# Kernel tuning notes

Hardware: AMD Instinct MI355X
Metric: run time of the kernel (lower is better)

Reference implementation:

```python
import jax, jax.numpy as jnp
import numpy as np

N = 50000   # nodes
D = 128     # hidden dim
E_NS = 250000  # non-self-loop edges
B = 4096    # sessions
NEG_SLOPE = 0.01  # F.leaky_relu default


def setup_inputs() -> dict:
    key = jax.random.key(0)
    ks = jax.random.split(key, 8)
    x = jax.random.normal(ks[0], (N, D), jnp.float32)
    src = jax.random.randint(ks[1], (E_NS,), 0, N)
    off = jax.random.randint(ks[2], (E_NS,), 1, N)
    dst = (src + off) % N  # guarantees src != dst
    loops = jnp.arange(N)
    edge_index = jnp.stack([jnp.concatenate([src, loops]),
                            jnp.concatenate([dst, loops])])  # [2, E_NS+N]
    batch = jnp.sort(jax.random.randint(ks[3], (N,), 0, B))
    local_sess_avg = jax.random.normal(ks[4], (B, D), jnp.float32)
    stdv = 1.0 / np.sqrt(D)
    W_alpha = jax.random.uniform(ks[5], (1, D), jnp.float32, -stdv, stdv)
    W_forward = jax.random.uniform(ks[6], (1, D), jnp.float32, -stdv, stdv)
    W_backward = jax.random.uniform(ks[7], (1, D), jnp.float32, -stdv, stdv)
    mt_sess_masks = jnp.ones((N,), jnp.int32)
    return {"x": x, "W_alpha": W_alpha, "W_forward": W_forward,
            "W_backward": W_backward, "local_sess_avg": local_sess_avg,
            "edge_index": edge_index, "batch": batch,
            "mt_sess_masks": mt_sess_masks, "n_nonself": E_NS}


def reference(x, W_alpha, W_forward, W_backward, local_sess_avg,
              edge_index, batch, mt_sess_masks, n_nonself):
    n = x.shape[0]
    src, dst = edge_index[0], edge_index[1]
    # non-self-loop edges occupy the first n_nonself columns (static int)
    src_ns, dst_ns = src[:n_nonself], dst[:n_nonself]
    # expanded edges = original edges + reversed non-self-loop edges
    exp_src = jnp.concatenate([src, dst_ns])  # [Et]
    exp_dst = jnp.concatenate([dst, src_ns])  # [Et]

    lrelu = lambda v: jax.nn.leaky_relu(v, NEG_SLOPE)

    exp_xi = x[exp_dst]                     # [Et, D]
    exp_xj = x[exp_src]                     # [Et, D]
    alpha_query = local_sess_avg[batch[exp_dst]]  # [Et, D]
    alpha = lrelu((exp_xi * alpha_query) @ W_alpha.T)        # [Et, 1]
    beta = lrelu((x[dst] * x[src]) @ W_forward.T)            # [E, 1]
    rbeta = lrelu((x[dst_ns] * x[src_ns]) @ W_backward.T)    # [E_ns, 1]
    logits = (jnp.concatenate([beta, rbeta], axis=0) + alpha)[:, 0]  # [Et]

    # segment softmax over target nodes (every node has a self-loop)
    seg_max = jax.lax.stop_gradient(
        jax.ops.segment_max(logits, exp_dst, num_segments=n))
    ex = jnp.exp(logits - seg_max[exp_dst])
    denom = jax.ops.segment_sum(ex, exp_dst, num_segments=n)
    aij = ex / denom[exp_dst]

    # scatter-add weighted neighbor features
    aggr = jax.ops.segment_sum(aij[:, None] * exp_xj, exp_dst, num_segments=n)

    # update: masked nodes take aggregate, others keep x; residual add
    new_x = jnp.where((mt_sess_masks == 1)[:, None], aggr, x)
    return new_x + x
```

## Files before the change

kernel.cpp:

```cpp
#include <hip/hip_runtime.h>

#define NEG_SLOPE 0.01f
#define STRIDE 32

__device__ __forceinline__ float lrelu(float v) { return v > 0.f ? v : NEG_SLOPE * v; }

__device__ __forceinline__ unsigned pack_bf16(float a, float b) {
    unsigned ua = __float_as_uint(a);
    ua = (ua + 0x7fffu + ((ua >> 16) & 1u)) >> 16;
    unsigned ub = __float_as_uint(b);
    ub = (ub + 0x7fffu + ((ub >> 16) & 1u)) & 0xffff0000u;
    return ua | ub;
}
__device__ __forceinline__ float blo(unsigned u) { return __uint_as_float(u << 16); }
__device__ __forceinline__ float bhi(unsigned u) { return __uint_as_float(u & 0xffff0000u); }

__device__ __forceinline__ void placeEdge(int s, int d, unsigned flag,
                                          int* __restrict__ cursor, int* __restrict__ slots) {
    int pos = atomicAdd(&cursor[d], 1);
    if (pos < STRIDE) slots[d * STRIDE + pos] = (int)((unsigned)s | flag);
}

__global__ void prep_kernel(const float4* __restrict__ x4, uint4* __restrict__ xh,
                            const int* __restrict__ EI0, const int* __restrict__ EI1,
                            int* __restrict__ cursor, int* __restrict__ slots,
                            int E_total, int E_NS, int nConvert) {
    int t = blockIdx.x * blockDim.x + threadIdx.x;
    if (t < nConvert) {
        float4 a = x4[2 * t], b = x4[2 * t + 1];
        uint4 o;
        o.x = pack_bf16(a.x, a.y);
        o.y = pack_bf16(a.z, a.w);
        o.z = pack_bf16(b.x, b.y);
        o.w = pack_bf16(b.z, b.w);
        xh[t] = o;
        return;
    }
    int u = t - nConvert;
    int n1v = E_total >> 2, n0v = E_NS >> 2;
    if (u < n1v) {
        int4 s = ((const int4*)EI0)[u];
        int4 d = ((const int4*)EI1)[u];
        placeEdge(s.x, d.x, 0u, cursor, slots);
        placeEdge(s.y, d.y, 0u, cursor, slots);
        placeEdge(s.z, d.z, 0u, cursor, slots);
        placeEdge(s.w, d.w, 0u, cursor, slots);
    } else if (u < n1v + n0v) {
        int v = u - n1v;
        int4 s = ((const int4*)EI1)[v];
        int4 d = ((const int4*)EI0)[v];
        placeEdge(s.x, d.x, 0x80000000u, cursor, slots);
        placeEdge(s.y, d.y, 0x80000000u, cursor, slots);
        placeEdge(s.z, d.z, 0x80000000u, cursor, slots);
        placeEdge(s.w, d.w, 0x80000000u, cursor, slots);
    } else if (u == n1v + n0v) {
        for (int e = E_total & ~3; e < E_total; e++)
            placeEdge(EI0[e], EI1[e], 0u, cursor, slots);
        for (int e = E_NS & ~3; e < E_NS; e++)
            placeEdge(EI1[e], EI0[e], 0x80000000u, cursor, slots);
    }
}

__device__ __forceinline__ float dot8u(uint4 h, float4 y0, float4 y1) {
    return blo(h.x) * y0.x + bhi(h.x) * y0.y + blo(h.y) * y0.z + bhi(h.y) * y0.w +
           blo(h.z) * y1.x + bhi(h.z) * y1.y + blo(h.w) * y1.z + bhi(h.w) * y1.w;
}

__global__ void gather_kernel(const float4* __restrict__ x4, const uint4* __restrict__ xh,
                              const float4* __restrict__ Wf4, const float4* __restrict__ Wb4,
                              const int* __restrict__ cursor, const int* __restrict__ slots,
                              const int* __restrict__ mask,
                              float4* __restrict__ out4, int N) {
    __shared__ int sbuck[16][STRIDE];
    int tid = blockIdx.x * blockDim.x + threadIdx.x;
    int node = tid >> 4;
    int sub = threadIdx.x & 15;
    int grp = threadIdx.x >> 4;
    bool active = (node < N);
    int nodeSafe = active ? node : 0;

    long long base = (long long)nodeSafe * 32;
    float4 xd0 = x4[base + 2 * sub];
    float4 xd1 = x4[base + 2 * sub + 1];
    int msk = active ? mask[nodeSafe] : 0;
    int cnt = (active && msk == 1) ? min(cursor[nodeSafe], STRIDE) : 0;

    if (sub < 8) ((int4*)sbuck[grp])[sub] = ((const int4*)slots)[(long long)nodeSafe * 8 + sub];

    float4 wf0 = Wf4[2 * sub], wf1 = Wf4[2 * sub + 1];
    float4 wb0 = Wb4[2 * sub], wb1 = Wb4[2 * sub + 1];
    float4 yf0 = {xd0.x * wf0.x, xd0.y * wf0.y, xd0.z * wf0.z, xd0.w * wf0.w};
    float4 yf1 = {xd1.x * wf1.x, xd1.y * wf1.y, xd1.z * wf1.z, xd1.w * wf1.w};
    float4 yb0 = {xd0.x * wb0.x, xd0.y * wb0.y, xd0.z * wb0.z, xd0.w * wb0.w};
    float4 yb1 = {xd1.x * wb1.x, xd1.y * wb1.y, xd1.z * wb1.z, xd1.w * wb1.w};

    int cm = cnt;
    cm = max(cm, __shfl_xor(cm, 16, 64));
    cm = max(cm, __shfl_xor(cm, 32, 64));

    float l = 0.f;
    float4 O0 = {0.f, 0.f, 0.f, 0.f}, O1 = {0.f, 0.f, 0.f, 0.f};

    for (int r = 0; r < cm; r += 8) {
        int e[8];
        uint4 h[8];
#pragma unroll
        for (int j = 0; j < 8; j++) {
            int i = r + j;
            e[j] = (i < cnt) ? sbuck[grp][i] : 0;
        }
#pragma unroll
        for (int j = 0; j < 8; j++)
            h[j] = xh[(long long)(e[j] & 0x7fffffff) * 16 + sub];

        float p[8];
#pragma unroll
        for (int j = 0; j < 8; j++) {
            float pf = dot8u(h[j], yf0, yf1);
            float pb = dot8u(h[j], yb0, yb1);
            p[j] = (e[j] < 0) ? pb : pf;
        }
#pragma unroll
        for (int sh = 1; sh < 16; sh <<= 1) {
#pragma unroll
            for (int j = 0; j < 8; j++) p[j] += __shfl_xor(p[j], sh, 64);
        }
#pragma unroll
        for (int j = 0; j < 8; j++) {
            float ev = (r + j < cnt) ? __expf(lrelu(p[j])) : 0.f;
            l += ev;
            O0.x += ev * blo(h[j].x); O0.y += ev * bhi(h[j].x);
            O0.z += ev * blo(h[j].y); O0.w += ev * bhi(h[j].y);
            O1.x += ev * blo(h[j].z); O1.y += ev * bhi(h[j].z);
            O1.z += ev * blo(h[j].w); O1.w += ev * bhi(h[j].w);
        }
    }

    if (active) {
        float4 ra, rb;
        if (msk == 1) {
            float inv = (l > 0.f) ? 1.f / l : 0.f;
            ra = {O0.x * inv + xd0.x, O0.y * inv + xd0.y, O0.z * inv + xd0.z, O0.w * inv + xd0.w};
            rb = {O1.x * inv + xd1.x, O1.y * inv + xd1.y, O1.z * inv + xd1.z, O1.w * inv + xd1.w};
        } else {
            ra = {2.f * xd0.x, 2.f * xd0.y, 2.f * xd0.z, 2.f * xd0.w};
            rb = {2.f * xd1.x, 2.f * xd1.y, 2.f * xd1.z, 2.f * xd1.w};
        }
        out4[base + 2 * sub] = ra;
        out4[base + 2 * sub + 1] = rb;
    }
}

extern "C" void kernel_launch(void* const* d_in, const int* in_sizes, int n_in,
                              void* d_out, int out_size, void* d_ws, size_t ws_size,
                              hipStream_t stream) {
    const float* x   = (const float*)d_in[0];
    const float* Wf  = (const float*)d_in[2];
    const float* Wb  = (const float*)d_in[3];
    const int* EI    = (const int*)d_in[5];
    const int* mask  = (const int*)d_in[7];

    int N = in_sizes[6];
    int E_total = in_sizes[5] / 2;
    int E_NS = E_total - N;

    const int* EI0 = EI;
    const int* EI1 = EI + E_total;

    char* ws = (char*)d_ws;
    int* cursor = (int*)ws;
    int* slots  = (int*)(ws + (size_t)N * 4);
    uint4* xh   = (uint4*)(ws + (size_t)N * 4 * (1 + STRIDE));

    hipMemsetAsync(cursor, 0, (size_t)N * 4, stream);

    const int BLK = 256;
    int nConvert = N * 16;
    int fillThreads = (E_total >> 2) + (E_NS >> 2) + 1;
    int prepBlocks = (nConvert + fillThreads + BLK - 1) / BLK;
    int nodeBlocks = ((N * 16) + BLK - 1) / BLK;

    prep_kernel<<<prepBlocks, BLK, 0, stream>>>((const float4*)x, xh, EI0, EI1,
                                                cursor, slots, E_total, E_NS, nConvert);
    gather_kernel<<<nodeBlocks, BLK, 0, stream>>>(
        (const float4*)x, (const uint4*)xh, (const float4*)Wf, (const float4*)Wb,
        cursor, slots, mask, (float4*)d_out, N);
}
```

Baseline: 160.6 us.

## Drop bf16 copy of x and gather fp32 rows directly in aggregation

```diff
diff --git a/kernel.cpp b/kernel.cpp
--- a/kernel.cpp
+++ b/kernel.cpp
@@ -5,68 +5,27 @@
 
 __device__ __forceinline__ float lrelu(float v) { return v > 0.f ? v : NEG_SLOPE * v; }
 
-__device__ __forceinline__ unsigned pack_bf16(float a, float b) {
-    unsigned ua = __float_as_uint(a);
-    ua = (ua + 0x7fffu + ((ua >> 16) & 1u)) >> 16;
-    unsigned ub = __float_as_uint(b);
-    ub = (ub + 0x7fffu + ((ub >> 16) & 1u)) & 0xffff0000u;
-    return ua | ub;
-}
-__device__ __forceinline__ float blo(unsigned u) { return __uint_as_float(u << 16); }
-__device__ __forceinline__ float bhi(unsigned u) { return __uint_as_float(u & 0xffff0000u); }
-
-__device__ __forceinline__ void placeEdge(int s, int d, unsigned flag,
-                                          int* __restrict__ cursor, int* __restrict__ slots) {
-    int pos = atomicAdd(&cursor[d], 1);
-    if (pos < STRIDE) slots[d * STRIDE + pos] = (int)((unsigned)s | flag);
+__device__ __forceinline__ float dot4(float4 a, float4 b) {
+    return a.x * b.x + a.y * b.y + a.z * b.z + a.w * b.w;
 }
 
-__global__ void prep_kernel(const float4* __restrict__ x4, uint4* __restrict__ xh,
-                            const int* __restrict__ EI0, const int* __restrict__ EI1,
+__global__ void fill_kernel(const int* __restrict__ EI0, const int* __restrict__ EI1,
                             int* __restrict__ cursor, int* __restrict__ slots,
-                            int E_total, int E_NS, int nConvert) {
+                            int E_total, int E_NS) {
     int t = blockIdx.x * blockDim.x + threadIdx.x;
-    if (t < nConvert) {
-        float4 a = x4[2 * t], b = x4[2 * t + 1];
-        uint4 o;
-        o.x = pack_bf16(a.x, a.y);
-        o.y = pack_bf16(a.z, a.w);
-        o.z = pack_bf16(b.x, b.y);
-        o.w = pack_bf16(b.z, b.w);
-        xh[t] = o;
-        return;
-    }
-    int u = t - nConvert;
-    int n1v = E_total >> 2, n0v = E_NS >> 2;
-    if (u < n1v) {
-        int4 s = ((const int4*)EI0)[u];
-        int4 d = ((const int4*)EI1)[u];
-        placeEdge(s.x, d.x, 0u, cursor, slots);
-        placeEdge(s.y, d.y, 0u, cursor, slots);
-        placeEdge(s.z, d.z, 0u, cursor, slots);
-        placeEdge(s.w, d.w, 0u, cursor, slots);
-    } else if (u < n1v + n0v) {
-        int v = u - n1v;
-        int4 s = ((const int4*)EI1)[v];
-        int4 d = ((const int4*)EI0)[v];
-        placeEdge(s.x, d.x, 0x80000000u, cursor, slots);
-        placeEdge(s.y, d.y, 0x80000000u, cursor, slots);
-        placeEdge(s.z, d.z, 0x80000000u, cursor, slots);
-        placeEdge(s.w, d.w, 0x80000000u, cursor, slots);
-    } else if (u == n1v + n0v) {
-        for (int e = E_total & ~3; e < E_total; e++)
-            placeEdge(EI0[e], EI1[e], 0u, cursor, slots);
-        for (int e = E_NS & ~3; e < E_NS; e++)
-            placeEdge(EI1[e], EI0[e], 0x80000000u, cursor, slots);
+    if (t < E_total) {
+        int s = EI0[t], d = EI1[t];
+        int pos = atomicAdd(&cursor[d], 1);
+        if (pos < STRIDE) slots[d * STRIDE + pos] = s;
+    } else if (t < E_total + E_NS) {
+        int e = t - E_total;
+        int s = EI1[e], d = EI0[e];
+        int pos = atomicAdd(&cursor[d], 1);
+        if (pos < STRIDE) slots[d * STRIDE + pos] = (int)((unsigned)s | 0x80000000u);
     }
 }
 
-__device__ __forceinline__ float dot8u(uint4 h, float4 y0, float4 y1) {
-    return blo(h.x) * y0.x + bhi(h.x) * y0.y + blo(h.y) * y0.z + bhi(h.y) * y0.w +
-           blo(h.z) * y1.x + bhi(h.z) * y1.y + blo(h.w) * y1.z + bhi(h.w) * y1.w;
-}
-
-__global__ void gather_kernel(const float4* __restrict__ x4, const uint4* __restrict__ xh,
+__global__ void gather_kernel(const float4* __restrict__ x4,
                               const float4* __restrict__ Wf4, const float4* __restrict__ Wb4,
                               const int* __restrict__ cursor, const int* __restrict__ slots,
                               const int* __restrict__ mask,
@@ -101,38 +60,41 @@
     float l = 0.f;
     float4 O0 = {0.f, 0.f, 0.f, 0.f}, O1 = {0.f, 0.f, 0.f, 0.f};
 
-    for (int r = 0; r < cm; r += 8) {
-        int e[8];
-        uint4 h[8];
+    for (int r = 0; r < cm; r += 4) {
+        int e[4];
+        float4 ra[4], rb[4];
 #pragma unroll
-        for (int j = 0; j < 8; j++) {
+        for (int j = 0; j < 4; j++) {
             int i = r + j;
             e[j] = (i < cnt) ? sbuck[grp][i] : 0;
         }
 #pragma unroll
-        for (int j = 0; j < 8; j++)
-            h[j] = xh[(long long)(e[j] & 0x7fffffff) * 16 + sub];
+        for (int j = 0; j < 4; j++) {
+            long long s = (long long)(e[j] & 0x7fffffff) * 32;
+            ra[j] = x4[s + 2 * sub];
+            rb[j] = x4[s + 2 * sub + 1];
+        }
 
-        float p[8];
+        float p[4];
 #pragma unroll
-        for (int j = 0; j < 8; j++) {
-            float pf = dot8u(h[j], yf0, yf1);
-            float pb = dot8u(h[j], yb0, yb1);
+        for (int j = 0; j < 4; j++) {
+            float pf = dot4(ra[j], yf0) + dot4(rb[j], yf1);
+            float pb = dot4(ra[j], yb0) + dot4(rb[j], yb1);
             p[j] = (e[j] < 0) ? pb : pf;
         }
 #pragma unroll
         for (int sh = 1; sh < 16; sh <<= 1) {
 #pragma unroll
-            for (int j = 0; j < 8; j++) p[j] += __shfl_xor(p[j], sh, 64);
+            for (int j = 0; j < 4; j++) p[j] += __shfl_xor(p[j], sh, 64);
         }
 #pragma unroll
-        for (int j = 0; j < 8; j++) {
+        for (int j = 0; j < 4; j++) {
             float ev = (r + j < cnt) ? __expf(lrelu(p[j])) : 0.f;
             l += ev;
-            O0.x += ev * blo(h[j].x); O0.y += ev * bhi(h[j].x);
-            O0.z += ev * blo(h[j].y); O0.w += ev * bhi(h[j].y);
-            O1.x += ev * blo(h[j].z); O1.y += ev * bhi(h[j].z);
-            O1.z += ev * blo(h[j].w); O1.w += ev * bhi(h[j].w);
+            O0.x += ev * ra[j].x; O0.y += ev * ra[j].y;
+            O0.z += ev * ra[j].z; O0.w += ev * ra[j].w;
+            O1.x += ev * rb[j].x; O1.y += ev * rb[j].y;
+            O1.z += ev * rb[j].z; O1.w += ev * rb[j].w;
         }
     }
 
@@ -170,19 +132,16 @@
     char* ws = (char*)d_ws;
     int* cursor = (int*)ws;
     int* slots  = (int*)(ws + (size_t)N * 4);
-    uint4* xh   = (uint4*)(ws + (size_t)N * 4 * (1 + STRIDE));
 
     hipMemsetAsync(cursor, 0, (size_t)N * 4, stream);
 
     const int BLK = 256;
-    int nConvert = N * 16;
-    int fillThreads = (E_total >> 2) + (E_NS >> 2) + 1;
-    int prepBlocks = (nConvert + fillThreads + BLK - 1) / BLK;
+    int fillThreads = E_total + E_NS;
+    int fillBlocks = (fillThreads + BLK - 1) / BLK;
     int nodeBlocks = ((N * 16) + BLK - 1) / BLK;
 
-    prep_kernel<<<prepBlocks, BLK, 0, stream>>>((const float4*)x, xh, EI0, EI1,
-                                                cursor, slots, E_total, E_NS, nConvert);
+    fill_kernel<<<fillBlocks, BLK, 0, stream>>>(EI0, EI1, cursor, slots, E_total, E_NS);
     gather_kernel<<<nodeBlocks, BLK, 0, stream>>>(
-        (const float4*)x, (const uint4*)xh, (const float4*)Wf, (const float4*)Wb,
+        (const float4*)x, (const float4*)Wf, (const float4*)Wb,
         cursor, slots, mask, (float4*)d_out, N);
 }
```

Result: no change. 160.4 us (-0.1%).
